# Performance work log

Hardware: AMD Instinct MI355X
Metric: run time of the kernel (lower is better)

The kernel has to match this reference:

```python
import jax, jax.numpy as jnp
import numpy as np
from math import sqrt

NUM_HEADS = 16
DIM_MODEL = 1024


def setup_inputs() -> dict:
    key = jax.random.key(0)
    ks = jax.random.split(key, 12)
    B, S, D, M = 4, 1024, DIM_MODEL, 64
    bound = 1.0 / sqrt(D)
    def lin_w(k):
        return jax.random.uniform(k, (D, D), jnp.float32, -bound, bound)
    def lin_b(k):
        return jax.random.uniform(k, (D,), jnp.float32, -bound, bound)
    return {
        "query": jax.random.normal(ks[0], (B, S, D), jnp.float32),
        "key": jax.random.normal(ks[1], (B, S, D), jnp.float32),
        "value": jax.random.normal(ks[2], (B, S, D), jnp.float32),
        "mask": jax.random.randint(ks[3], (1, B, S, M), 0, 2).astype(jnp.float32),
        "Wq": lin_w(ks[4]), "bq": lin_b(ks[5]),
        "Wk": lin_w(ks[6]), "bk": lin_b(ks[7]),
        "Wv": lin_w(ks[8]), "bv": lin_b(ks[9]),
        "Wo": lin_w(ks[10]),
    }


def reference(query, key, value, mask, Wq, bq, Wk, bk, Wv, bv, Wo):
    B, S, D = query.shape
    H = NUM_HEADS
    d = D // H
    # projections + head split, permute(2,0,1,3) -> [H,B,S,d]
    q = (query @ Wq.T + bq).reshape(B, S, H, d).transpose(2, 0, 1, 3)
    k = (key @ Wk.T + bk).reshape(B, S, H, d).transpose(2, 0, 1, 3)
    v = (value @ Wv.T + bv).reshape(B, S, H, d).transpose(2, 0, 1, 3)
    attn = jnp.einsum("hbqd,hbkd->hbqk", q, k) / sqrt(d)  # [H,B,S,S]
    # custom mask: mask.repeat(H,1,1,1) then mask @ mask^T / sqrt(m).
    # Identical per-head, so compute once on [B,S,m] and broadcast over H.
    m2d = mask[0]  # [B,S,m]
    mm = jnp.einsum("bqm,bkm->bqk", m2d, m2d) / sqrt(m2d.shape[-1])
    attn = jnp.where(mm[None] == 0, jnp.float32(-1e9), attn)
    w = jax.nn.softmax(attn, axis=-1)  # dropout is identity in eval mode
    x = jnp.einsum("hbqk,hbkd->hbqd", w, v)  # [H,B,S,d]
    # torch: permute(1,2,0,3) -> [B,S,H,d]; transpose(1,2) -> [B,H,S,d];
    # contiguous().view(B,-1,H*d) -- row-major reshape (mixes head/seq layout, replicated faithfully)
    x = jnp.transpose(x, (1, 0, 2, 3))  # [B,H,S,d]
    x = x.reshape(B, -1, H * d)
    return x @ Wo.T
```

## Files before the change

kernel.cpp:

```cpp
#include <hip/hip_runtime.h>

typedef unsigned int u32;
typedef unsigned short u16;
typedef unsigned long long u64;
typedef __attribute__((ext_vector_type(8))) short s16x8;
typedef __attribute__((ext_vector_type(8))) __bf16 bf16x8;
typedef __attribute__((ext_vector_type(4))) float f32x4;
typedef __attribute__((ext_vector_type(16))) float f32x16;
typedef __attribute__((ext_vector_type(4))) u32 u32x4;

#define WSMB (1ull << 20)
#define QSC 0.18033688011112042f

static __device__ __forceinline__ u16 f2bf(float f) {
  u32 u = __builtin_bit_cast(u32, f);
  return (u16)((u + 0x7fffu + ((u >> 16) & 1u)) >> 16);
}

static __device__ __forceinline__ u32 pkbf(float lo, float hi) {
  u32 r;
  asm("v_cvt_pk_bf16_f32 %0, %1, %2" : "=v"(r) : "v"(lo), "v"(hi));
  return r;
}

static __device__ __forceinline__ float ex2(float x) {
  float r;
  asm("v_exp_f32 %0, %1" : "=v"(r) : "v"(x));
  return r;
}

static __device__ __forceinline__ f32x4 mfma16x16(s16x8 a, s16x8 b, f32x4 c) {
  return __builtin_amdgcn_mfma_f32_16x16x32_bf16(
      __builtin_bit_cast(bf16x8, a), __builtin_bit_cast(bf16x8, b), c, 0, 0, 0);
}

static __device__ __forceinline__ f32x16 mfma32x32(s16x8 a, s16x8 b, f32x16 c) {
  return __builtin_amdgcn_mfma_f32_32x32x16_bf16(
      __builtin_bit_cast(bf16x8, a), __builtin_bit_cast(bf16x8, b), c, 0, 0, 0);
}

#define GLOAD_LDS16(g, l)                                                      \
  __builtin_amdgcn_global_load_lds(                                            \
      (const __attribute__((address_space(1))) u32*)(const void*)(g),          \
      (__attribute__((address_space(3))) u32*)(void*)(l), 16, 0, 0)

__global__ __launch_bounds__(256) void k_prep(
    const float* __restrict__ xq, const float* __restrict__ xk,
    const float* __restrict__ xv, const float* __restrict__ wq,
    const float* __restrict__ wk, const float* __restrict__ wv,
    const float* __restrict__ wo, const float* __restrict__ mask,
    u16* __restrict__ oxq, u16* __restrict__ oxk, u16* __restrict__ oxv,
    u16* __restrict__ owq, u16* __restrict__ owk, u16* __restrict__ owv,
    u16* __restrict__ owo, u64* __restrict__ bits) {
  const int bid = blockIdx.x;
  if (bid >= 16384) {
    int w = threadIdx.x >> 6, l = threadIdx.x & 63;
    int r = (bid - 16384) * 4 + w;
    float v = mask[(size_t)r * 64 + l];
    u64 bl = __ballot(v != 0.0f);
    if (l == 0) bits[r] = bl;
    return;
  }
  const float* s;
  u16* d;
  int x;
  if (bid < 12288) {
    const int y = bid >> 12;
    x = bid & 4095;
    if (y == 0) { s = xq; d = oxq; }
    else if (y == 1) { s = xk; d = oxk; }
    else { s = xv; d = oxv; }
  } else {
    const int y = (bid - 12288) >> 10;
    x = (bid - 12288) & 1023;
    if (y == 0) { s = wq; d = owq; }
    else if (y == 1) { s = wk; d = owk; }
    else if (y == 2) { s = wv; d = owv; }
    else { s = wo; d = owo; }
  }
  int i = (x * 256 + threadIdx.x) * 4;
  float4 v = *(const float4*)(s + i);
  u64 p = (u64)f2bf(v.x) | ((u64)f2bf(v.y) << 16) | ((u64)f2bf(v.z) << 32) |
          ((u64)f2bf(v.w) << 48);
  *(u64*)(d + i) = p;
}

static __device__ __forceinline__ void gemm_core(const u16* __restrict__ A,
                                                 const u16* __restrict__ Bw,
                                                 f32x4 (&acc)[4][4]) {
  __shared__ __attribute__((aligned(16))) u16 As[2][4096];
  __shared__ __attribute__((aligned(16))) u16 Bs[2][4096];
  const int t = threadIdx.x;
  const int l = t & 63, w = t >> 6, lr = l & 15, lk = l >> 4;
  const int amr = (w & 1) * 64, bnr = (w >> 1) * 64;
  const int c0 = t, c1 = t + 256;
  const int r0 = c0 >> 2, r1 = c1 >> 2;
  const int sw0 = ((c0 & 3) * 8) ^ ((r0 & 6) << 2);
  const int sw1 = ((c1 & 3) * 8) ^ ((r1 & 6) << 2);
  const u16* Ag0 = A + (size_t)r0 * 1024 + sw0;
  const u16* Ag1 = A + (size_t)r1 * 1024 + sw1;
  const u16* Bg0 = Bw + (size_t)r0 * 1024 + sw0;
  const u16* Bg1 = Bw + (size_t)r1 * 1024 + sw1;
  const int aswz = (lk * 16) ^ ((lr & 6) << 3);

  GLOAD_LDS16(Ag0, &As[0][c0 * 8]);
  GLOAD_LDS16(Ag1, &As[0][c1 * 8]);
  GLOAD_LDS16(Bg0, &Bs[0][c0 * 8]);
  GLOAD_LDS16(Bg1, &Bs[0][c1 * 8]);

  int cur = 0;
  for (int kt = 0; kt < 1024; kt += 32) {
    __syncthreads();
    if (kt < 992) {
      const int nxt = cur ^ 1;
      GLOAD_LDS16(Ag0 + kt + 32, &As[nxt][c0 * 8]);
      GLOAD_LDS16(Ag1 + kt + 32, &As[nxt][c1 * 8]);
      GLOAD_LDS16(Bg0 + kt + 32, &Bs[nxt][c0 * 8]);
      GLOAD_LDS16(Bg1 + kt + 32, &Bs[nxt][c1 * 8]);
    }
    const char* Ac = (const char*)As[cur];
    const char* Bc = (const char*)Bs[cur];
    s16x8 af[4], bf[4];
#pragma unroll
    for (int i = 0; i < 4; i++)
      af[i] = *(const s16x8*)(Ac + (amr + i * 16 + lr) * 64 + aswz);
#pragma unroll
    for (int j = 0; j < 4; j++)
      bf[j] = *(const s16x8*)(Bc + (bnr + j * 16 + lr) * 64 + aswz);
    __builtin_amdgcn_s_setprio(1);
#pragma unroll
    for (int i = 0; i < 4; i++)
#pragma unroll
      for (int j = 0; j < 4; j++)
        acc[i][j] = mfma16x16(af[i], bf[j], acc[i][j]);
    __builtin_amdgcn_s_setprio(0);
    cur ^= 1;
  }
}

static __device__ __forceinline__ void gemm_core64(const u16* __restrict__ A,
                                                   const u16* __restrict__ Bw,
                                                   f32x4 (&acc)[4][2]) {
  __shared__ __attribute__((aligned(16))) u16 As[2][4096];
  __shared__ __attribute__((aligned(16))) u16 Bs[2][2048];
  const int t = threadIdx.x;
  const int l = t & 63, w = t >> 6, lr = l & 15, lk = l >> 4;
  const int amr = (w & 1) * 64, bnr = (w >> 1) * 32;
  const int c0 = t, c1 = t + 256;
  const int r0 = c0 >> 2, r1 = c1 >> 2;
  const int sw0 = ((c0 & 3) * 8) ^ ((r0 & 6) << 2);
  const int sw1 = ((c1 & 3) * 8) ^ ((r1 & 6) << 2);
  const u16* Ag0 = A + (size_t)r0 * 1024 + sw0;
  const u16* Ag1 = A + (size_t)r1 * 1024 + sw1;
  const u16* Bg0 = Bw + (size_t)r0 * 1024 + sw0;
  const int aswz = (lk * 16) ^ ((lr & 6) << 3);

  GLOAD_LDS16(Ag0, &As[0][c0 * 8]);
  GLOAD_LDS16(Ag1, &As[0][c1 * 8]);
  GLOAD_LDS16(Bg0, &Bs[0][c0 * 8]);

  int cur = 0;
  for (int kt = 0; kt < 1024; kt += 32) {
    __syncthreads();
    if (kt < 992) {
      const int nxt = cur ^ 1;
      GLOAD_LDS16(Ag0 + kt + 32, &As[nxt][c0 * 8]);
      GLOAD_LDS16(Ag1 + kt + 32, &As[nxt][c1 * 8]);
      GLOAD_LDS16(Bg0 + kt + 32, &Bs[nxt][c0 * 8]);
    }
    const char* Ac = (const char*)As[cur];
    const char* Bc = (const char*)Bs[cur];
    s16x8 af[4], bf[2];
#pragma unroll
    for (int i = 0; i < 4; i++)
      af[i] = *(const s16x8*)(Ac + (amr + i * 16 + lr) * 64 + aswz);
#pragma unroll
    for (int j = 0; j < 2; j++)
      bf[j] = *(const s16x8*)(Bc + (bnr + j * 16 + lr) * 64 + aswz);
    __builtin_amdgcn_s_setprio(1);
#pragma unroll
    for (int i = 0; i < 4; i++)
#pragma unroll
      for (int j = 0; j < 2; j++)
        acc[i][j] = mfma16x16(af[i], bf[j], acc[i][j]);
    __builtin_amdgcn_s_setprio(0);
    cur ^= 1;
  }
}

__global__ __launch_bounds__(256) void k_qkv(
    const u16* __restrict__ Xq, const u16* __restrict__ Xk,
    const u16* __restrict__ Xv, const u16* __restrict__ Wqb,
    const u16* __restrict__ Wkb, const u16* __restrict__ Wvb,
    const float* __restrict__ bq, const float* __restrict__ bk,
    const float* __restrict__ bv, u16* __restrict__ Qo, u16* __restrict__ Ko,
    u16* __restrict__ V4, const u64* __restrict__ bits,
    u64* __restrict__ MB) {
  const int bid0 = blockIdx.x;
  if (bid0 >= 768) {
    int wv = threadIdx.x >> 6, l = threadIdx.x & 63;
    int qg = (bid0 - 768) * 4 + wv;
    u64 bqw = bits[qg];
    const u64* bb = bits + (qg & ~1023);
    u64* out = MB + (size_t)qg * 16;
    for (int kt = 0; kt < 16; kt++) {
      u64 bkw = bb[kt * 64 + l];
      u64 m = __ballot((bqw & bkw) != 0ull);
      if (l == 0) out[kt] = m;
    }
    return;
  }
  const int bid = (bid0 & 7) * 96 + (bid0 >> 3);
  const int proj = bid >> 8;
  const int rem = bid & 255;
  const int st = rem >> 3, dt = rem & 7;
  const u16* Xp = proj == 0 ? Xq : (proj == 1 ? Xk : Xv);
  const u16* Wp = proj == 0 ? Wqb : (proj == 1 ? Wkb : Wvb);
  const float* bias = proj == 0 ? bq : (proj == 1 ? bk : bv);
  const int t = threadIdx.x;
  const int l = t & 63, w = t >> 6, lr = l & 15, lk = l >> 4;
  const int amr = (w & 1) * 64, bnr = (w >> 1) * 64;
  f32x4 acc[4][4] = {};
  if (proj < 2) {
    const float sc = proj == 0 ? QSC : 1.0f;
    gemm_core(Wp + (size_t)dt * 131072, Xp + (size_t)st * 131072, acc);
    u16* O = proj ? Ko : Qo;
#pragma unroll
    for (int i = 0; i < 4; i++) {
      const int d0 = dt * 128 + amr + i * 16 + lk * 4;
      const int h = d0 >> 6, dd0 = d0 & 63;
      const float4 b4 = *(const float4*)(bias + d0);
#pragma unroll
      for (int j = 0; j < 4; j++) {
        const int s = st * 128 + bnr + j * 16 + lr;
        const int b_ = s >> 10, si = s & 1023;
        u32 e0 = pkbf((acc[i][j][0] + b4.x) * sc, (acc[i][j][1] + b4.y) * sc);
        u32 e1 = pkbf((acc[i][j][2] + b4.z) * sc, (acc[i][j][3] + b4.w) * sc);
        *(u64*)(O + ((size_t)((b_ * 16 + h) * 1024 + si)) * 64 + dd0) =
            (u64)e0 | ((u64)e1 << 32);
      }
    }
  } else {
    gemm_core(Xp + (size_t)st * 131072, Wp + (size_t)dt * 131072, acc);
#pragma unroll
    for (int i = 0; i < 4; i++) {
      const int s0 = st * 128 + amr + i * 16 + lk * 4;
      const int b_ = s0 >> 10, si = s0 & 1023;
      const int sblk = si >> 3, soff = si & 7;
#pragma unroll
      for (int j = 0; j < 4; j++) {
        const int d = dt * 128 + bnr + j * 16 + lr;
        const int h = d >> 6, dd = d & 63;
        const float bb = bias[d];
        u32 e0 = pkbf(acc[i][j][0] + bb, acc[i][j][1] + bb);
        u32 e1 = pkbf(acc[i][j][2] + bb, acc[i][j][3] + bb);
        *(u64*)(V4 + (size_t)(b_ * 16 + h) * 65536 +
                (size_t)(sblk * 64 + dd) * 8 + soff) =
            (u64)e0 | ((u64)e1 << 32);
      }
    }
  }
}

__global__ __launch_bounds__(256) void k_oproj(const u16* __restrict__ Xb,
                                               const u16* __restrict__ Wob,
                                               float* __restrict__ Out) {
  const int bid0 = blockIdx.x;
  const int bid = (bid0 & 7) * 64 + (bid0 >> 3);
  const int mb = bid >> 4, nb = bid & 15;
  f32x4 acc[4][2] = {};
  gemm_core64(Xb + (size_t)mb * 131072, Wob + (size_t)nb * 65536, acc);
  const int t = threadIdx.x;
  const int l = t & 63, w = t >> 6, lr = l & 15, lk = l >> 4;
  const int amr = (w & 1) * 64, bnr = (w >> 1) * 32;
#pragma unroll
  for (int i = 0; i < 4; i++)
#pragma unroll
    for (int j = 0; j < 2; j++)
#pragma unroll
      for (int r = 0; r < 4; r++) {
        const int m = mb * 128 + amr + i * 16 + lk * 4 + r;
        const int n = nb * 64 + bnr + j * 16 + lr;
        Out[(size_t)m * 1024 + n] = acc[i][j][r];
      }
}

__global__ __launch_bounds__(256, 3) void k_attn(const u16* __restrict__ Qb,
                                                 const u16* __restrict__ Kb,
                                                 const u16* __restrict__ V4,
                                                 const u64* __restrict__ MB,
                                                 u16* __restrict__ xbuf) {
  __shared__ __attribute__((aligned(16))) u16 Ks[2][4096];
  __shared__ __attribute__((aligned(16))) u16 Vs[2][4096];
  const int t = threadIdx.x, l = t & 63, w = t >> 6;
  const int q5 = l & 31, hi = l >> 5;
  const int bid = (blockIdx.x & 7) * 64 + (blockIdx.x >> 3);
  const int qt = bid & 7, hb = bid >> 3;
  const int h = hb >> 2, b = hb & 3;
  const int s0 = qt * 128;
  const u16* Qhb = Qb + (size_t)(b * 16 + h) * 65536;
  const u16* Khb = Kb + (size_t)(b * 16 + h) * 65536;
  const u16* Vhb = V4 + (size_t)(b * 16 + h) * 65536;
  const int q = s0 + w * 32 + q5;
  const u64* MBq = MB + ((size_t)b * 1024 + q) * 16;

  s16x8 qf[4];
#pragma unroll
  for (int ds = 0; ds < 4; ds++)
    qf[ds] = *(const s16x8*)(Qhb + (size_t)q * 64 + ds * 16 + hi * 8);

  f32x16 xa0 = {}, xa1 = {};
  float ls = 0.f, m_ = -__builtin_inff();

  const int ca = t, cb_ = t + 256;
  const int rA = ca >> 3, colA = (ca & 7) * 16;
  const int rB = cb_ >> 3, colB = (cb_ & 7) * 16;
  const int sA = colA ^ ((rA & 7) << 4);
  const int sB = colB ^ ((rB & 7) << 4);
  const u16* KgA = Khb + (size_t)rA * 64 + (sA >> 1);
  const u16* KgB = Khb + (size_t)rB * 64 + (sB >> 1);
  const u16* VgA = Vhb + (size_t)(sA >> 4) * 512 + rA * 8;
  const u16* VgB = Vhb + (size_t)(sB >> 4) * 512 + rB * 8;

  const int rbase = q5 * 128 + ((hi * 16) ^ ((q5 & 7) << 4));

  GLOAD_LDS16(KgA, &Ks[0][ca * 8]);
  GLOAD_LDS16(KgB, &Ks[0][cb_ * 8]);
  GLOAD_LDS16(VgA, &Vs[0][ca * 8]);
  GLOAD_LDS16(VgB, &Vs[0][cb_ * 8]);
  u64 mw = MBq[0];

  int cur = 0;
  for (int kt = 0; kt < 16; kt++) {
    __syncthreads();
    if (kt < 15) {
      const int nxt = cur ^ 1;
      GLOAD_LDS16(KgA + (kt + 1) * 4096, &Ks[nxt][ca * 8]);
      GLOAD_LDS16(KgB + (kt + 1) * 4096, &Ks[nxt][cb_ * 8]);
      GLOAD_LDS16(VgA + (kt + 1) * 4096, &Vs[nxt][ca * 8]);
      GLOAD_LDS16(VgB + (kt + 1) * 4096, &Vs[nxt][cb_ * 8]);
    }
    const u64 nw = MBq[(kt + 1) & 15];
    const char* Kc = (const char*)Ks[cur];
    const char* Vc = (const char*)Vs[cur];

    f32x16 z0 = {}, z1 = {};
#pragma unroll
    for (int ds = 0; ds < 4; ds++) {
      s16x8 k0 = *(const s16x8*)(Kc + (rbase ^ (ds * 32)));
      s16x8 k1 = *(const s16x8*)(Kc + 4096 + (rbase ^ (ds * 32)));
      __builtin_amdgcn_s_setprio(1);
      z0 = mfma32x32(k0, qf[ds], z0);
      z1 = mfma32x32(k1, qf[ds], z1);
      __builtin_amdgcn_s_setprio(0);
    }

    float tmx[16];
#pragma unroll
    for (int r = 0; r < 16; r++) tmx[r] = fmaxf(z0[r], z1[r]);
#pragma unroll
    for (int st_ = 8; st_ >= 1; st_ >>= 1)
#pragma unroll
      for (int r = 0; r < 8; r++)
        if (r < st_) tmx[r] = fmaxf(tmx[r], tmx[r + st_]);
    float tm = tmx[0];
    tm = fmaxf(tm, __shfl_xor(tm, 32));
    if (tm > m_) {
      const float scl = ex2(m_ - tm);
      m_ = tm;
      ls *= scl;
      xa0 *= scl;
      xa1 *= scl;
    }

    float e0[16], e1[16];
#pragma unroll
    for (int r = 0; r < 16; r++) e0[r] = ex2(z0[r] - m_);
#pragma unroll
    for (int r = 0; r < 16; r++) e1[r] = ex2(z1[r] - m_);
    if (!__all(mw == ~0ull)) {
      const u32 mh0 = (u32)(mw >> (hi * 4));
      const u32 mh1 = (u32)(mw >> (hi * 4 + 32));
#pragma unroll
      for (int r = 0; r < 16; r++) {
        const int bp = 8 * (r >> 2) + (r & 3);
        e0[r] = ((mh0 >> bp) & 1u) ? e0[r] : 0.f;
        e1[r] = ((mh1 >> bp) & 1u) ? e1[r] : 0.f;
      }
    }
    float ts = 0.f;
#pragma unroll
    for (int r = 0; r < 16; r++) ts += e0[r] + e1[r];
    ls += ts;

    u32 P0[2][4], P1[2][4];
#pragma unroll
    for (int qi = 0; qi < 4; qi++) {
      P0[0][qi] = pkbf(e0[4 * qi], e0[4 * qi + 1]);
      P1[0][qi] = pkbf(e0[4 * qi + 2], e0[4 * qi + 3]);
      P0[1][qi] = pkbf(e1[4 * qi], e1[4 * qi + 1]);
      P1[1][qi] = pkbf(e1[4 * qi + 2], e1[4 * qi + 3]);
    }

#pragma unroll
    for (int ks = 0; ks < 4; ks++) {
      const int kb = ks >> 1, qi0 = (ks & 1) * 2, qi1 = qi0 + 1;
      u32 w0 = P0[kb][qi0], w2 = P0[kb][qi1];
      u32 w1 = P1[kb][qi0], w3 = P1[kb][qi1];
      asm("v_permlane32_swap_b32 %0, %1" : "+v"(w0), "+v"(w2));
      asm("v_permlane32_swap_b32 %0, %1" : "+v"(w1), "+v"(w3));
      u32x4 fv;
      fv[0] = w0; fv[1] = w1; fv[2] = w2; fv[3] = w3;
      const s16x8 pb = __builtin_bit_cast(s16x8, fv);
      s16x8 v0 = *(const s16x8*)(Vc + (rbase ^ (ks * 32)));
      s16x8 v1 = *(const s16x8*)(Vc + 4096 + (rbase ^ (ks * 32)));
      __builtin_amdgcn_s_setprio(1);
      xa0 = mfma32x32(v0, pb, xa0);
      xa1 = mfma32x32(v1, pb, xa1);
      __builtin_amdgcn_s_setprio(0);
    }
    mw = nw;
    cur ^= 1;
  }

  ls += __shfl_xor(ls, 32);
  const float inv = 1.0f / ls;
  const size_t rowb = (size_t)b * 1048576 + (size_t)(h * 64 + (q >> 4)) * 1024 +
                      (size_t)(q & 15) * 64;
#pragma unroll
  for (int qi = 0; qi < 4; qi++) {
    u32 a0 = pkbf(xa0[4 * qi] * inv, xa0[4 * qi + 1] * inv);
    u32 a1 = pkbf(xa0[4 * qi + 2] * inv, xa0[4 * qi + 3] * inv);
    *(u64*)(xbuf + rowb + 8 * qi + 4 * hi) = (u64)a0 | ((u64)a1 << 32);
    u32 b0 = pkbf(xa1[4 * qi] * inv, xa1[4 * qi + 1] * inv);
    u32 b1 = pkbf(xa1[4 * qi + 2] * inv, xa1[4 * qi + 3] * inv);
    *(u64*)(xbuf + rowb + 32 + 8 * qi + 4 * hi) = (u64)b0 | ((u64)b1 << 32);
  }
}

extern "C" void kernel_launch(void* const* d_in, const int* in_sizes, int n_in,
                              void* d_out, int out_size, void* d_ws,
                              size_t ws_size, hipStream_t stream) {
  const float* query = (const float*)d_in[0];
  const float* key_ = (const float*)d_in[1];
  const float* value = (const float*)d_in[2];
  const float* mask = (const float*)d_in[3];
  const float* bq = (const float*)d_in[5];
  const float* bk = (const float*)d_in[7];
  const float* bv = (const float*)d_in[9];
  const float* Wq = (const float*)d_in[4];
  const float* Wk = (const float*)d_in[6];
  const float* Wv = (const float*)d_in[8];
  const float* Wo = (const float*)d_in[10];

  char* ws = (char*)d_ws;
  u16* Xq = (u16*)(ws + 0 * WSMB);
  u16* Xk = (u16*)(ws + 8 * WSMB);
  u16* Xv = (u16*)(ws + 16 * WSMB);
  u16* Wqb = (u16*)(ws + 24 * WSMB);
  u16* Wkb = (u16*)(ws + 26 * WSMB);
  u16* Wvb = (u16*)(ws + 28 * WSMB);
  u16* Wob = (u16*)(ws + 30 * WSMB);
  u16* Qb = (u16*)(ws + 32 * WSMB);
  u16* Kb = (u16*)(ws + 40 * WSMB);
  u16* V4 = (u16*)(ws + 48 * WSMB);
  u64* bits = (u64*)(ws + 56 * WSMB);
  u64* MBm = (u64*)(ws + 57 * WSMB);
  u16* xbuf = Xq;

  k_prep<<<17408, 256, 0, stream>>>(query, key_, value, Wq, Wk, Wv, Wo, mask,
                                    Xq, Xk, Xv, Wqb, Wkb, Wvb, Wob, bits);
  k_qkv<<<1792, 256, 0, stream>>>(Xq, Xk, Xv, Wqb, Wkb, Wvb, bq, bk, bv, Qb,
                                  Kb, V4, bits, MBm);
  k_attn<<<512, 256, 0, stream>>>(Qb, Kb, V4, MBm, xbuf);
  k_oproj<<<512, 256, 0, stream>>>(xbuf, Wob, (float*)d_out);
}
```

Measured before the change: 114.9 us.

## Split key range across two warp groups in attention and merge via LDS

Doubles the attention block to 512 threads: two warp groups each process half of the key tiles for the same 128 queries, with their own double-buffered K/V in shared memory. At the end, the second group writes its partial accumulators, max and sum to shared memory, and the first group merges them with an online-softmax rescale. The change also flattens the row-max reduction into four independent chains. It shortens the serial key loop per wave and increases waves per CU, at the cost of doubled shared memory and a final combine step.

```diff
diff --git a/kernel.cpp b/kernel.cpp
--- a/kernel.cpp
+++ b/kernel.cpp
@@ -285,15 +285,17 @@
       }
 }
 
-__global__ __launch_bounds__(256, 3) void k_attn(const u16* __restrict__ Qb,
+__global__ __launch_bounds__(512, 2) void k_attn(const u16* __restrict__ Qb,
                                                  const u16* __restrict__ Kb,
                                                  const u16* __restrict__ V4,
                                                  const u64* __restrict__ MB,
                                                  u16* __restrict__ xbuf) {
-  __shared__ __attribute__((aligned(16))) u16 Ks[2][4096];
-  __shared__ __attribute__((aligned(16))) u16 Vs[2][4096];
+  __shared__ __attribute__((aligned(16))) u16 Ks[2][2][4096];
+  __shared__ __attribute__((aligned(16))) u16 Vs[2][2][4096];
   const int t = threadIdx.x, l = t & 63, w = t >> 6;
   const int q5 = l & 31, hi = l >> 5;
+  const int wq = w & 3;
+  const int kh = w >> 2;
   const int bid = (blockIdx.x & 7) * 64 + (blockIdx.x >> 3);
   const int qt = bid & 7, hb = bid >> 3;
   const int h = hb >> 2, b = hb & 3;
@@ -301,8 +303,9 @@
   const u16* Qhb = Qb + (size_t)(b * 16 + h) * 65536;
   const u16* Khb = Kb + (size_t)(b * 16 + h) * 65536;
   const u16* Vhb = V4 + (size_t)(b * 16 + h) * 65536;
-  const int q = s0 + w * 32 + q5;
+  const int q = s0 + wq * 32 + q5;
   const u64* MBq = MB + ((size_t)b * 1024 + q) * 16;
+  const int kt0 = kh * 8;
 
   s16x8 qf[4];
 #pragma unroll
@@ -312,37 +315,32 @@
   f32x16 xa0 = {}, xa1 = {};
   float ls = 0.f, m_ = -__builtin_inff();
 
-  const int ca = t, cb_ = t + 256;
-  const int rA = ca >> 3, colA = (ca & 7) * 16;
-  const int rB = cb_ >> 3, colB = (cb_ & 7) * 16;
-  const int sA = colA ^ ((rA & 7) << 4);
-  const int sB = colB ^ ((rB & 7) << 4);
-  const u16* KgA = Khb + (size_t)rA * 64 + (sA >> 1);
-  const u16* KgB = Khb + (size_t)rB * 64 + (sB >> 1);
-  const u16* VgA = Vhb + (size_t)(sA >> 4) * 512 + rA * 8;
-  const u16* VgB = Vhb + (size_t)(sB >> 4) * 512 + rB * 8;
+  const int rS = t >> 3, colS = (t & 7) * 16;
+  const int sS = colS ^ ((rS & 7) << 4);
+  const u16* Kg = Khb + (size_t)rS * 64 + (sS >> 1);
+  const u16* Vg = Vhb + (size_t)(sS >> 4) * 512 + rS * 8;
 
   const int rbase = q5 * 128 + ((hi * 16) ^ ((q5 & 7) << 4));
 
-  GLOAD_LDS16(KgA, &Ks[0][ca * 8]);
-  GLOAD_LDS16(KgB, &Ks[0][cb_ * 8]);
-  GLOAD_LDS16(VgA, &Vs[0][ca * 8]);
-  GLOAD_LDS16(VgB, &Vs[0][cb_ * 8]);
-  u64 mw = MBq[0];
+  GLOAD_LDS16(Kg + 0 * 4096, &Ks[0][0][t * 8]);
+  GLOAD_LDS16(Kg + 8 * 4096, &Ks[0][1][t * 8]);
+  GLOAD_LDS16(Vg + 0 * 4096, &Vs[0][0][t * 8]);
+  GLOAD_LDS16(Vg + 8 * 4096, &Vs[0][1][t * 8]);
+  u64 mw = MBq[kt0];
 
   int cur = 0;
-  for (int kt = 0; kt < 16; kt++) {
+  for (int i = 0; i < 8; i++) {
     __syncthreads();
-    if (kt < 15) {
+    if (i < 7) {
       const int nxt = cur ^ 1;
-      GLOAD_LDS16(KgA + (kt + 1) * 4096, &Ks[nxt][ca * 8]);
-      GLOAD_LDS16(KgB + (kt + 1) * 4096, &Ks[nxt][cb_ * 8]);
-      GLOAD_LDS16(VgA + (kt + 1) * 4096, &Vs[nxt][ca * 8]);
-      GLOAD_LDS16(VgB + (kt + 1) * 4096, &Vs[nxt][cb_ * 8]);
-    }
-    const u64 nw = MBq[(kt + 1) & 15];
-    const char* Kc = (const char*)Ks[cur];
-    const char* Vc = (const char*)Vs[cur];
+      GLOAD_LDS16(Kg + (i + 1) * 4096, &Ks[nxt][0][t * 8]);
+      GLOAD_LDS16(Kg + (9 + i) * 4096, &Ks[nxt][1][t * 8]);
+      GLOAD_LDS16(Vg + (i + 1) * 4096, &Vs[nxt][0][t * 8]);
+      GLOAD_LDS16(Vg + (9 + i) * 4096, &Vs[nxt][1][t * 8]);
+    }
+    const u64 nw = MBq[kt0 + ((i + 1) & 7)];
+    const char* Kc = (const char*)Ks[cur][kh];
+    const char* Vc = (const char*)Vs[cur][kh];
 
     f32x16 z0 = {}, z1 = {};
 #pragma unroll
@@ -355,15 +353,16 @@
       __builtin_amdgcn_s_setprio(0);
     }
 
-    float tmx[16];
-#pragma unroll
-    for (int r = 0; r < 16; r++) tmx[r] = fmaxf(z0[r], z1[r]);
-#pragma unroll
-    for (int st_ = 8; st_ >= 1; st_ >>= 1)
-#pragma unroll
-      for (int r = 0; r < 8; r++)
-        if (r < st_) tmx[r] = fmaxf(tmx[r], tmx[r + st_]);
-    float tm = tmx[0];
+    float t0 = fmaxf(z0[0], z1[0]), t1 = fmaxf(z0[1], z1[1]);
+    float t2 = fmaxf(z0[2], z1[2]), t3 = fmaxf(z0[3], z1[3]);
+#pragma unroll
+    for (int r = 4; r < 16; r += 4) {
+      t0 = fmaxf(t0, fmaxf(z0[r], z1[r]));
+      t1 = fmaxf(t1, fmaxf(z0[r + 1], z1[r + 1]));
+      t2 = fmaxf(t2, fmaxf(z0[r + 2], z1[r + 2]));
+      t3 = fmaxf(t3, fmaxf(z0[r + 3], z1[r + 3]));
+    }
+    float tm = fmaxf(fmaxf(t0, t1), fmaxf(t2, t3));
     tm = fmaxf(tm, __shfl_xor(tm, 32));
     if (tm > m_) {
       const float scl = ex2(m_ - tm);
@@ -373,40 +372,39 @@
       xa1 *= scl;
     }
 
-    float e0[16], e1[16];
-#pragma unroll
-    for (int r = 0; r < 16; r++) e0[r] = ex2(z0[r] - m_);
-#pragma unroll
-    for (int r = 0; r < 16; r++) e1[r] = ex2(z1[r] - m_);
+#pragma unroll
+    for (int r = 0; r < 16; r++) z0[r] = ex2(z0[r] - m_);
+#pragma unroll
+    for (int r = 0; r < 16; r++) z1[r] = ex2(z1[r] - m_);
     if (!__all(mw == ~0ull)) {
       const u32 mh0 = (u32)(mw >> (hi * 4));
       const u32 mh1 = (u32)(mw >> (hi * 4 + 32));
 #pragma unroll
       for (int r = 0; r < 16; r++) {
         const int bp = 8 * (r >> 2) + (r & 3);
-        e0[r] = ((mh0 >> bp) & 1u) ? e0[r] : 0.f;
-        e1[r] = ((mh1 >> bp) & 1u) ? e1[r] : 0.f;
+        z0[r] = ((mh0 >> bp) & 1u) ? z0[r] : 0.f;
+        z1[r] = ((mh1 >> bp) & 1u) ? z1[r] : 0.f;
       }
     }
     float ts = 0.f;
 #pragma unroll
-    for (int r = 0; r < 16; r++) ts += e0[r] + e1[r];
+    for (int r = 0; r < 16; r++) ts += z0[r] + z1[r];
     ls += ts;
 
     u32 P0[2][4], P1[2][4];
 #pragma unroll
     for (int qi = 0; qi < 4; qi++) {
-      P0[0][qi] = pkbf(e0[4 * qi], e0[4 * qi + 1]);
-      P1[0][qi] = pkbf(e0[4 * qi + 2], e0[4 * qi + 3]);
-      P0[1][qi] = pkbf(e1[4 * qi], e1[4 * qi + 1]);
-      P1[1][qi] = pkbf(e1[4 * qi + 2], e1[4 * qi + 3]);
+      P0[0][qi] = pkbf(z0[4 * qi], z0[4 * qi + 1]);
+      P1[0][qi] = pkbf(z0[4 * qi + 2], z0[4 * qi + 3]);
+      P0[1][qi] = pkbf(z1[4 * qi], z1[4 * qi + 1]);
+      P1[1][qi] = pkbf(z1[4 * qi + 2], z1[4 * qi + 3]);
     }
 
 #pragma unroll
     for (int ks = 0; ks < 4; ks++) {
-      const int kb = ks >> 1, qi0 = (ks & 1) * 2, qi1 = qi0 + 1;
-      u32 w0 = P0[kb][qi0], w2 = P0[kb][qi1];
-      u32 w1 = P1[kb][qi0], w3 = P1[kb][qi1];
+      const int kb_ = ks >> 1, qi0 = (ks & 1) * 2, qi1 = qi0 + 1;
+      u32 w0 = P0[kb_][qi0], w2 = P0[kb_][qi1];
+      u32 w1 = P1[kb_][qi0], w3 = P1[kb_][qi1];
       asm("v_permlane32_swap_b32 %0, %1" : "+v"(w0), "+v"(w2));
       asm("v_permlane32_swap_b32 %0, %1" : "+v"(w1), "+v"(w3));
       u32x4 fv;
@@ -421,6 +419,29 @@
     }
     mw = nw;
     cur ^= 1;
+  }
+
+  float* cmb = (float*)&Ks[0][0][0];
+  __syncthreads();
+  if (w >= 4) {
+    float* p = &cmb[(size_t)((w - 4) * 64 + l) * 36];
+    *(f32x16*)(p) = xa0;
+    *(f32x16*)(p + 16) = xa1;
+    p[32] = m_;
+    p[33] = ls;
+  }
+  __syncthreads();
+  if (w >= 4) return;
+  {
+    const float* p = &cmb[(size_t)(wq * 64 + l) * 36];
+    const f32x16 xb0 = *(const f32x16*)(p);
+    const f32x16 xb1 = *(const f32x16*)(p + 16);
+    const float mb = p[32], lsb = p[33];
+    const float m = fmaxf(m_, mb);
+    const float sa = ex2(m_ - m), sb = ex2(mb - m);
+    ls = ls * sa + lsb * sb;
+    xa0 = xa0 * sa + xb0 * sb;
+    xa1 = xa1 * sa + xb1 * sb;
   }
 
   ls += __shfl_xor(ls, 32);
@@ -472,6 +493,6 @@
                                     Xq, Xk, Xv, Wqb, Wkb, Wvb, Wob, bits);
   k_qkv<<<1792, 256, 0, stream>>>(Xq, Xk, Xv, Wqb, Wkb, Wvb, bq, bk, bv, Qb,
                                   Kb, V4, bits, MBm);
-  k_attn<<<512, 256, 0, stream>>>(Qb, Kb, V4, MBm, xbuf);
+  k_attn<<<512, 512, 0, stream>>>(Qb, Kb, V4, MBm, xbuf);
   k_oproj<<<512, 256, 0, stream>>>(xbuf, Wob, (float*)d_out);
 }
```

Result: no change. 115.2 us (median of 2 runs) (+0.3%).
